# Kernel tuning notes

Measured on AMD Instinct MI355X. Metric: run time of the kernel, lower is better.

Reference implementation:

```python
import jax, jax.numpy as jnp
import numpy as np

EMBED_DIM = 256
HEADS = 8
HEAD_DIM = EMBED_DIM // HEADS
T = 8            # time grid points
N0, N1 = 32, 32  # spatial grid
MAX_PATCH = 16   # static slot budget per cell (last slot = grid latent token)
NEG = -1e30


def construct_grid():
    g0 = jnp.linspace(0.0, 1.0, N0)
    g1 = jnp.linspace(0.0, 1.0, N1)
    G0, G1 = jnp.meshgrid(g0, g1, indexing='ij')
    return jnp.stack([G0, G1], axis=-1)  # [N0, N1, 2]


def setup_inputs() -> dict:
    key = jax.random.key(0)
    ks = jax.random.split(key, 8)
    m, n = 4, 16384
    x = jax.random.uniform(ks[0], (m, n, 3))                       # coords: (time, s0, s1) in [0,1]
    z = jax.random.normal(ks[1], (m, n, EMBED_DIM))
    time_grid = jnp.tile(jnp.linspace(0.0, 1.0, T)[None], (m, 1))  # [m, T] uniform time grid
    latents = jax.random.normal(ks[2], (N0, N1, EMBED_DIM))
    grid = construct_grid()
    s = 1.0 / np.sqrt(EMBED_DIM)
    Wq = jax.random.normal(ks[3], (EMBED_DIM, EMBED_DIM)) * s
    Wk = jax.random.normal(ks[4], (EMBED_DIM, EMBED_DIM)) * s
    Wv = jax.random.normal(ks[5], (EMBED_DIM, EMBED_DIM)) * s
    Wo = jax.random.normal(ks[6], (EMBED_DIM, EMBED_DIM)) * s
    return {'x': x, 'z': z, 'time_grid': time_grid, 'latents': latents,
            'grid': grid, 'Wq': Wq, 'Wk': Wk, 'Wv': Wv, 'Wo': Wo}


def _cumcount(idx):
    # idx: [n] int; returns per-element count of prior occurrences of the same value
    n = idx.shape[0]
    order = jnp.argsort(idx)                 # stable
    srt = idx[order]
    ar = jnp.arange(n)
    is_start = jnp.concatenate([jnp.array([True]), srt[1:] != srt[:-1]])
    seg_start = jax.lax.cummax(jnp.where(is_start, ar, 0), axis=0)
    cc = ar - seg_start
    return jnp.zeros_like(idx).at[order].set(cc.astype(idx.dtype))


def _forward(x, z, time_grid, latents, grid, Wq, Wk, Wv, Wo):
    m, n, _ = x.shape
    t = time_grid.shape[1]
    S = t * N0 * N1
    # --- build x_grid: repeat spatial grid over (m,t), insert time coord at dim 0 ---
    xg_sp = jnp.broadcast_to(grid[None, None], (m, t, N0, N1, 2))
    tg = jnp.broadcast_to(time_grid[:, :, None, None, None], (m, t, N0, N1, 1))
    x_grid = jnp.concatenate([tg, xg_sp], axis=-1)          # [m,t,N0,N1,3]
    # --- nearest gridded neighbour (k=1): per-dim rounding on the regular grid ---
    grid_shape = jnp.array([t, N0, N1], jnp.float32)
    xg_flat = x_grid.reshape(m, S, 3)
    xmin = xg_flat.min(axis=1)                               # [m,3]
    xmax = xg_flat.max(axis=1)
    spacing = (xmax - xmin) / (grid_shape - 1.0)             # [m,3]
    multi = jnp.floor((x - xmin[:, None] + spacing[:, None] / 2) / spacing[:, None])
    multi = jnp.clip(multi, 0.0, grid_shape - 1.0)
    strides = jnp.array([N0 * N1, N1, 1], jnp.float32)
    nearest = jnp.sum(multi * strides, axis=-1).astype(jnp.int32)  # [m,n] flat cell id
    # --- per-cell slot allocation via cumulative count ---
    cum = jax.vmap(_cumcount)(nearest)                       # [m,n]
    P = MAX_PATCH
    valid = cum < (P - 1)                                    # last slot reserved for grid token
    bidx = jnp.arange(m)[:, None]
    cell = jnp.where(valid, nearest, S)                      # out-of-bounds -> dropped
    slot = jnp.minimum(cum, P - 2)
    # --- scatter points into the joint grid [m, S, P, E]; slot P-1 = grid latent ---
    joint = jnp.zeros((m, S, P, EMBED_DIM), z.dtype)
    joint = joint.at[bidx, cell, slot].set(z, mode='drop')
    z_grid_flat = jnp.broadcast_to(
        latents.reshape(1, 1, N0 * N1, EMBED_DIM), (m, t, N0 * N1, EMBED_DIM)
    ).reshape(m, S, EMBED_DIM)
    joint = joint.at[:, :, P - 1].set(z_grid_flat)
    counts = jnp.zeros((m, S), jnp.int32).at[bidx, cell].add(1, mode='drop')
    counts = jnp.minimum(counts, P - 1)
    att_mask = jnp.concatenate(
        [jnp.arange(P - 1)[None, None] < counts[..., None],
         jnp.ones((m, S, 1), bool)], axis=-1)                # [m,S,P]
    # --- masked multi-head cross attention: 1 query (grid latent) per cell ---
    q = (z_grid_flat @ Wq).reshape(m, S, HEADS, HEAD_DIM)
    k = (joint @ Wk).reshape(m, S, P, HEADS, HEAD_DIM)
    v = (joint @ Wv).reshape(m, S, P, HEADS, HEAD_DIM)
    logits = jnp.einsum('mshd,msphd->mshp', q, k) / np.sqrt(HEAD_DIM)
    logits = jnp.where(att_mask[:, :, None, :], logits, NEG)
    attn = jax.nn.softmax(logits, axis=-1)
    out = jnp.einsum('mshp,msphd->mshd', attn, v).reshape(m, S, EMBED_DIM) @ Wo
    z_grid = out.reshape(m, t, N0, N1, EMBED_DIM)
    return x_grid, z_grid


def reference(x, z, time_grid, latents, grid, Wq, Wk, Wv, Wo):
    return _forward(x, z, time_grid, latents, grid, Wq, Wk, Wv, Wo)
```

## Files before the change

### kernel.cpp

```cpp
#include <hip/hip_runtime.h>
#include <hip/hip_bf16.h>

#define T_ 8
#define N0_ 32
#define N1_ 32
#define SP_ (N0_*N1_)
#define S_ (T_*SP_)
#define E_ 256
#define P_ 16
#define NH_ 8
#define HD_ 32

typedef __attribute__((ext_vector_type(8))) short short8;
typedef __attribute__((ext_vector_type(4))) float f32x4;
typedef __attribute__((ext_vector_type(8))) unsigned short u16x8;

__device__ __forceinline__ unsigned short f2bf(float f) {
  __hip_bfloat16 h = __float2bfloat16(f);
  return *reinterpret_cast<unsigned short*>(&h);
}
__device__ __forceinline__ float bf2f(unsigned short u) {
  return __uint_as_float((unsigned)u << 16);
}

__device__ __forceinline__ void gl_lds16(const void* g, void* l) {
  __builtin_amdgcn_global_load_lds(
      (const __attribute__((address_space(1))) unsigned int*)(g),
      (__attribute__((address_space(3))) unsigned int*)(l), 16, 0, 0);
}

__global__ __launch_bounds__(256) void prep(const float* __restrict__ z,
                                            unsigned short* __restrict__ z16,
                                            const float* __restrict__ x,
                                            const float* __restrict__ tg,
                                            const float* __restrict__ grid,
                                            float* __restrict__ out,
                                            int* __restrict__ counts,
                                            int* __restrict__ cell_raw,
                                            const float* __restrict__ Wq,
                                            const float* __restrict__ Wk,
                                            const float* __restrict__ Wv,
                                            const float* __restrict__ Wo,
                                            unsigned short* __restrict__ wT,
                                            const float* __restrict__ latents,
                                            unsigned short* __restrict__ lat16,
                                            int m, int n, int tot_xg, int zn8) {
  __shared__ float ts[64][65];
  __shared__ float st[4][6];
  int bid = blockIdx.x;
  int tid = threadIdx.x;
  if (bid < 2048) {
    for (int i = bid * 256 + tid; i < zn8; i += 2048 * 256) {
      float4 a = *(const float4*)(z + (size_t)i * 8);
      float4 b = *(const float4*)(z + (size_t)i * 8 + 4);
      u16x8 o;
      o[0]=f2bf(a.x); o[1]=f2bf(a.y); o[2]=f2bf(a.z); o[3]=f2bf(a.w);
      o[4]=f2bf(b.x); o[5]=f2bf(b.y); o[6]=f2bf(b.z); o[7]=f2bf(b.w);
      *(u16x8*)(z16 + (size_t)i * 8) = o;
    }
    return;
  }
  if (bid < 2304) {
    if (tid < 64) {
      float mn0 = 1e30f, mx0 = -1e30f, mn1 = 1e30f, mx1 = -1e30f;
      for (int i = tid; i < SP_; i += 64) {
        float g0 = grid[i*2], g1 = grid[i*2+1];
        mn0 = fminf(mn0, g0); mx0 = fmaxf(mx0, g0);
        mn1 = fminf(mn1, g1); mx1 = fmaxf(mx1, g1);
      }
      for (int msk = 32; msk; msk >>= 1) {
        mn0 = fminf(mn0, __shfl_xor(mn0, msk));
        mx0 = fmaxf(mx0, __shfl_xor(mx0, msk));
        mn1 = fminf(mn1, __shfl_xor(mn1, msk));
        mx1 = fmaxf(mx1, __shfl_xor(mx1, msk));
      }
      if (tid == 0) {
        for (int b = 0; b < m; ++b) {
          float tmn = 1e30f, tmx = -1e30f;
          for (int tt = 0; tt < T_; ++tt) {
            float v = tg[b*T_ + tt];
            tmn = fminf(tmn, v); tmx = fmaxf(tmx, v);
          }
          st[b][0] = tmn; st[b][1] = mn0; st[b][2] = mn1;
          st[b][3] = (tmx - tmn) / (float)(T_ - 1);
          st[b][4] = (mx0 - mn0) / (float)(N0_ - 1);
          st[b][5] = (mx1 - mn1) / (float)(N1_ - 1);
        }
      }
    }
    __syncthreads();
    int idx = (bid - 2048) * 256 + tid;
    if (idx < tot_xg) {
      int sp = idx & (SP_ - 1);
      int bt = idx >> 10;
      out[idx*3 + 0] = tg[bt];
      out[idx*3 + 1] = grid[sp*2 + 0];
      out[idx*3 + 2] = grid[sp*2 + 1];
    }
    if (idx < m*n) {
      int b = idx / n;
      int j = idx - b*n;
      const float* s = st[b];
      float xt = x[(size_t)idx*3 + 0], x0 = x[(size_t)idx*3 + 1], x1 = x[(size_t)idx*3 + 2];
      float m0 = floorf((xt - s[0] + s[3]*0.5f) / s[3]);
      float m1 = floorf((x0 - s[1] + s[4]*0.5f) / s[4]);
      float m2 = floorf((x1 - s[2] + s[5]*0.5f) / s[5]);
      m0 = fminf(fmaxf(m0, 0.f), (float)(T_ - 1));
      m1 = fminf(fmaxf(m1, 0.f), (float)(N0_ - 1));
      m2 = fminf(fmaxf(m2, 0.f), (float)(N1_ - 1));
      int sc = (int)m0 * SP_ + (int)m1 * N1_ + (int)m2;
      int cg = b * S_ + sc;
      int old = atomicAdd(&counts[cg], 1);
      if (old < P_) cell_raw[(size_t)cg * P_ + old] = j;
    }
    return;
  }
  if (bid < 2368) {
    int wb = bid - 2304;
    int mat = wb >> 4;
    int tile = wb & 15;
    int tr = (tile >> 2) * 64;
    int tc = (tile & 3) * 64;
    const float* W = mat == 0 ? Wq : mat == 1 ? Wk : mat == 2 ? Wv : Wo;
    int r = tid >> 2, c0 = (tid & 3) * 16;
#pragma unroll
    for (int i = 0; i < 4; ++i) {
      float4 v = *(const float4*)&W[(size_t)(tr + r) * 256 + tc + c0 + i*4];
      ts[r][c0 + i*4 + 0] = v.x; ts[r][c0 + i*4 + 1] = v.y;
      ts[r][c0 + i*4 + 2] = v.z; ts[r][c0 + i*4 + 3] = v.w;
    }
    __syncthreads();
    u16x8 o0, o1;
#pragma unroll
    for (int i = 0; i < 8; ++i) o0[i] = f2bf(ts[c0 + i][r]);
#pragma unroll
    for (int i = 0; i < 8; ++i) o1[i] = f2bf(ts[c0 + 8 + i][r]);
    unsigned short* dst = wT + (size_t)(mat * 256 + tc + r) * 256 + tr + c0;
    *(u16x8*)dst = o0;
    *(u16x8*)(dst + 8) = o1;
    return;
  }
  for (int i = (bid - 2368) * 256 + tid; i < SP_ * E_ / 8; i += 16 * 256) {
    float4 a = *(const float4*)(latents + (size_t)i * 8);
    float4 b = *(const float4*)(latents + (size_t)i * 8 + 4);
    u16x8 o;
    o[0]=f2bf(a.x); o[1]=f2bf(a.y); o[2]=f2bf(a.z); o[3]=f2bf(a.w);
    o[4]=f2bf(b.x); o[5]=f2bf(b.y); o[6]=f2bf(b.z); o[7]=f2bf(b.w);
    *(u16x8*)(lat16 + (size_t)i * 8) = o;
  }
}

template <typename OutT>
__device__ __forceinline__ void g2l_body(unsigned short* __restrict__ ldsbuf,
                                         const unsigned short* __restrict__ A,
                                         const unsigned short* __restrict__ BT,
                                         OutT* __restrict__ C,
                                         int CP, int ldc, int L, int tid) {
  int rp = L / CP, cp = L - rp * CP;

  int wid = tid >> 6, lane = tid & 63, l15 = lane & 15, slot = lane >> 4;
  int wr = (wid >> 1) * 64, wc = (wid & 1) * 64;

  int r8 = lane >> 3, k8 = lane & 7;
  int colsw = (k8 ^ r8) << 3;
  const unsigned short* ga0 = A  + (size_t)(rp * 128 + wid * 32 + r8) * 256 + colsw;
  const unsigned short* gb0 = BT + (size_t)(cp * 128 + wid * 32 + r8) * 256 + colsw;
  unsigned short* As = ldsbuf;
  unsigned short* Bs = ldsbuf + 8192;

  f32x4 acc[4][4] = {};

#pragma unroll
  for (int kt = 0; kt < 4; ++kt) {
    const unsigned short* ga = ga0 + kt * 64;
    const unsigned short* gb = gb0 + kt * 64;
    gl_lds16(ga,          As + (wid*32     ) * 64);
    gl_lds16(ga +  8*256, As + (wid*32 +  8) * 64);
    gl_lds16(ga + 16*256, As + (wid*32 + 16) * 64);
    gl_lds16(ga + 24*256, As + (wid*32 + 24) * 64);
    gl_lds16(gb,          Bs + (wid*32     ) * 64);
    gl_lds16(gb +  8*256, Bs + (wid*32 +  8) * 64);
    gl_lds16(gb + 16*256, Bs + (wid*32 + 16) * 64);
    gl_lds16(gb + 24*256, Bs + (wid*32 + 24) * 64);
    asm volatile("s_waitcnt vmcnt(0)" ::: "memory");
    __builtin_amdgcn_s_barrier();
    asm volatile("" ::: "memory");
#pragma unroll
    for (int kf = 0; kf < 2; ++kf) {
      short8 afr[4], bfr[4];
      int sx = (kf * 4 + slot) ^ (l15 & 7);
#pragma unroll
      for (int mm = 0; mm < 4; ++mm) {
        int row = wr + mm * 16 + l15;
        afr[mm] = *(const short8*)&As[row * 64 + (sx << 3)];
      }
#pragma unroll
      for (int nn = 0; nn < 4; ++nn) {
        int col = wc + nn * 16 + l15;
        bfr[nn] = *(const short8*)&Bs[col * 64 + (sx << 3)];
      }
#pragma unroll
      for (int mm = 0; mm < 4; ++mm)
#pragma unroll
        for (int nn = 0; nn < 4; ++nn)
          acc[mm][nn] = __builtin_amdgcn_mfma_f32_16x16x32_bf16(afr[mm], bfr[nn], acc[mm][nn], 0, 0, 0);
    }
    asm volatile("" ::: "memory");
    __builtin_amdgcn_s_barrier();
    asm volatile("" ::: "memory");
  }

#pragma unroll
  for (int mm = 0; mm < 4; ++mm) {
#pragma unroll
    for (int nn = 0; nn < 4; ++nn) {
      int grow0 = rp * 128 + wr + mm * 16 + slot * 4;
      int gcol  = cp * 128 + wc + nn * 16 + l15;
#pragma unroll
      for (int j = 0; j < 4; ++j) {
        size_t o = (size_t)(grow0 + j) * ldc + gcol;
        if constexpr (__is_same(OutT, float)) C[o] = acc[mm][nn][j];
        else                                  C[o] = __float2bfloat16(acc[mm][nn][j]);
      }
    }
  }
}

__global__ __launch_bounds__(256, 3) void phase2(const unsigned short* __restrict__ z16,
                                                 const unsigned short* __restrict__ wT,
                                                 __hip_bfloat16* __restrict__ kv,
                                                 const unsigned short* __restrict__ lat16,
                                                 float* __restrict__ lat,
                                                 const int* __restrict__ counts,
                                                 int* __restrict__ cell_raw,
                                                 int* __restrict__ pts2, int total) {
  __shared__ unsigned short lds[2 * 128 * 64];
  int bid = blockIdx.x;
  if (bid < 2048) {
    int L = (bid & 7) * 256 + (bid >> 3);
    g2l_body<__hip_bfloat16>(lds, z16, wT + (size_t)256*256, kv, 4, 512, L, threadIdx.x);
    return;
  }
  if (bid < 2096) {
    g2l_body<float>(lds, lat16, wT, lat, 6, 768, bid - 2048, threadIdx.x);
    return;
  }
  int cg = (bid - 2096) * 256 + threadIdx.x;
  if (cg >= total) return;
  int cnt = counts[cg];
  int stored = cnt < P_ ? cnt : P_;
  int eff = cnt < (P_ - 1) ? cnt : (P_ - 1);
  int* p = cell_raw + (size_t)cg * P_;
  for (int i = 1; i < stored; ++i) {
    int key = p[i]; int j = i - 1;
    while (j >= 0 && p[j] > key) { p[j+1] = p[j]; --j; }
    p[j+1] = key;
  }
  int* o = pts2 + (size_t)cg * P_;
  o[0] = eff;
  for (int i = 0; i < eff; ++i) o[1 + i] = p[i];
}

template <typename OutT>
__global__ __launch_bounds__(256, 3) void gemm_g2l(const unsigned short* __restrict__ A,
                                                   const unsigned short* __restrict__ BT,
                                                   OutT* __restrict__ C,
                                                   int CP, int ldc) {
  __shared__ unsigned short lds[2 * 128 * 64];
  int nb = gridDim.x, bid = blockIdx.x;
  int L = bid;
  if ((nb & 7) == 0) L = (bid & 7) * (nb >> 3) + (bid >> 3);
  g2l_body<OutT>(lds, A, BT, C, CP, ldc, L, threadIdx.x);
}

__global__ __launch_bounds__(256) void attn_kernel(
    const float* __restrict__ lat,
    const __hip_bfloat16* __restrict__ kv,
    const int* __restrict__ pts2,
    __hip_bfloat16* __restrict__ attn_out, int n) {
  const float scale = 0.17677669529663687f;
  int wid = threadIdx.x >> 6;
  int lane = threadIdx.x & 63;
  int cellg = blockIdx.x * 4 + wid;
  int b = cellg >> 13;
  int c = cellg & (SP_ - 1);
  int d0 = lane << 2;

  const int* pp = pts2 + (size_t)cellg * P_;
  int4 h0 = *(const int4*)pp;
  int eff = h0.x;

  const float* latc = lat + c * 768 + d0;
  float4 q  = *(const float4*)latc;
  float4 kl = *(const float4*)(latc + 256);
  float4 vl = *(const float4*)(latc + 512);

  float p15 = q.x*kl.x + q.y*kl.y + q.z*kl.z + q.w*kl.w;
  p15 += __shfl_xor(p15, 1);
  p15 += __shfl_xor(p15, 2);
  p15 += __shfl_xor(p15, 4);
  float e15 = __expf(p15 * scale);
  float ssum = e15;
  float4 acc;
  acc.x = e15 * vl.x; acc.y = e15 * vl.y; acc.z = e15 * vl.z; acc.w = e15 * vl.w;

  const unsigned short* kvp = (const unsigned short*)kv;
  size_t bbase = (size_t)b * n;

  int pt[4]; pt[0] = h0.y; pt[1] = h0.z; pt[2] = h0.w; pt[3] = 0;
  int done = 0, cap = 3;
  while (done < eff) {
    int np = eff - done; if (np > cap) np = cap;
    ushort4 kr[4], vr[4];
#pragma unroll
    for (int i = 0; i < 4; ++i) if (i < np) {
      size_t row = (bbase + (size_t)pt[i]) * 512;
      kr[i] = *(const ushort4*)(kvp + row + d0);
      vr[i] = *(const ushort4*)(kvp + row + 256 + d0);
    }
    float e[4];
#pragma unroll
    for (int i = 0; i < 4; ++i) if (i < np) {
      float p = q.x*bf2f(kr[i].x) + q.y*bf2f(kr[i].y) + q.z*bf2f(kr[i].z) + q.w*bf2f(kr[i].w);
      p += __shfl_xor(p, 1);
      p += __shfl_xor(p, 2);
      p += __shfl_xor(p, 4);
      e[i] = __expf(p * scale);
    }
#pragma unroll
    for (int i = 0; i < 4; ++i) if (i < np) {
      ssum += e[i];
      acc.x += e[i] * bf2f(vr[i].x);
      acc.y += e[i] * bf2f(vr[i].y);
      acc.z += e[i] * bf2f(vr[i].z);
      acc.w += e[i] * bf2f(vr[i].w);
    }
    done += np;
    cap = 4;
    if (done < eff) {
      int4 h = *(const int4*)(pp + 1 + done);
      pt[0] = h.x; pt[1] = h.y; pt[2] = h.z; pt[3] = h.w;
    }
  }
  float inv = 1.f / ssum;
  ushort4 o;
  o.x = f2bf(acc.x * inv); o.y = f2bf(acc.y * inv);
  o.z = f2bf(acc.z * inv); o.w = f2bf(acc.w * inv);
  *(ushort4*)((unsigned short*)attn_out + (size_t)cellg * E_ + d0) = o;
}

extern "C" void kernel_launch(void* const* d_in, const int* in_sizes, int n_in,
                              void* d_out, int out_size, void* d_ws, size_t ws_size,
                              hipStream_t stream) {
  const float* x       = (const float*)d_in[0];
  const float* z       = (const float*)d_in[1];
  const float* tg      = (const float*)d_in[2];
  const float* latents = (const float*)d_in[3];
  const float* grid    = (const float*)d_in[4];
  const float* Wq      = (const float*)d_in[5];
  const float* Wk      = (const float*)d_in[6];
  const float* Wv      = (const float*)d_in[7];
  const float* Wo      = (const float*)d_in[8];

  int m = in_sizes[2] / T_;
  int n = in_sizes[1] / (m * E_);
  int MS = m * S_;
  float* out = (float*)d_out;
  int tot_xg = m * T_ * SP_;

  char* w = (char*)d_ws;
  auto alloc = [&](size_t bytes) { char* p = w; w += (bytes + 255) & ~(size_t)255; return p; };
  int*   counts     = (int*)  alloc((size_t)MS * 4);
  int*   cell_raw   = (int*)  alloc((size_t)MS * P_ * 4);
  int*   pts2       = (int*)  alloc((size_t)MS * P_ * 4);
  unsigned short* wT    = (unsigned short*)alloc((size_t)1024 * 256 * 2);
  unsigned short* lat16 = (unsigned short*)alloc((size_t)SP_ * E_ * 2);
  float* lat        = (float*)alloc((size_t)SP_ * 768 * 4);
  __hip_bfloat16* kv       = (__hip_bfloat16*)alloc((size_t)m * n * 512 * 2);
  __hip_bfloat16* attn_out = (__hip_bfloat16*)alloc((size_t)MS * E_ * 2);

  unsigned short* z16 = (unsigned short*)(out + (size_t)tot_xg * 3);

  (void)hipMemsetAsync(counts, 0, (size_t)MS * 4, stream);

  prep<<<2384, 256, 0, stream>>>(z, z16, x, tg, grid, out, counts, cell_raw,
                                 Wq, Wk, Wv, Wo, wT, latents, lat16,
                                 m, n, tot_xg, m * n * E_ / 8);

  phase2<<<2224, 256, 0, stream>>>(z16, wT, kv, lat16, lat, counts, cell_raw, pts2, MS);

  attn_kernel<<<MS/4, 256, 0, stream>>>(lat, kv, pts2, attn_out, n);

  gemm_g2l<float><<<512, 256, 0, stream>>>(
      (const unsigned short*)attn_out, wT + (size_t)768*256, out + (size_t)tot_xg * 3, 2, 256);
}
```

Baseline: 90.95 us.

## Fuse fp32-to-bf16 conversion of z and latents into the projection GEMM loads

Removes the separate pass that converted z (64 MB fp32) and latents to bf16 in the prep kernel. The K/V and latent projection GEMM now loads fp32 A tiles straight into LDS with a swizzled layout and converts them to bf16 in registers before the MFMAs. This saves one full write and re-read of the bf16 copy of z. In exchange the GEMM reads twice as many A bytes, uses more LDS (48KB), and does conversion ALU work in the inner loop with no double buffering.

New measurement: 83.46 us, median of 3. 8.2% less time.

```diff
diff --git a/kernel.cpp b/kernel.cpp
--- a/kernel.cpp
+++ b/kernel.cpp
@@ -29,9 +29,7 @@
       (__attribute__((address_space(3))) unsigned int*)(l), 16, 0, 0);
 }
 
-__global__ __launch_bounds__(256) void prep(const float* __restrict__ z,
-                                            unsigned short* __restrict__ z16,
-                                            const float* __restrict__ x,
+__global__ __launch_bounds__(256) void prep(const float* __restrict__ x,
                                             const float* __restrict__ tg,
                                             const float* __restrict__ grid,
                                             float* __restrict__ out,
@@ -42,25 +40,12 @@
                                             const float* __restrict__ Wv,
                                             const float* __restrict__ Wo,
                                             unsigned short* __restrict__ wT,
-                                            const float* __restrict__ latents,
-                                            unsigned short* __restrict__ lat16,
-                                            int m, int n, int tot_xg, int zn8) {
+                                            int m, int n, int tot_xg) {
   __shared__ float ts[64][65];
   __shared__ float st[4][6];
   int bid = blockIdx.x;
   int tid = threadIdx.x;
-  if (bid < 2048) {
-    for (int i = bid * 256 + tid; i < zn8; i += 2048 * 256) {
-      float4 a = *(const float4*)(z + (size_t)i * 8);
-      float4 b = *(const float4*)(z + (size_t)i * 8 + 4);
-      u16x8 o;
-      o[0]=f2bf(a.x); o[1]=f2bf(a.y); o[2]=f2bf(a.z); o[3]=f2bf(a.w);
-      o[4]=f2bf(b.x); o[5]=f2bf(b.y); o[6]=f2bf(b.z); o[7]=f2bf(b.w);
-      *(u16x8*)(z16 + (size_t)i * 8) = o;
-    }
-    return;
-  }
-  if (bid < 2304) {
+  if (bid < 256) {
     if (tid < 64) {
       float mn0 = 1e30f, mx0 = -1e30f, mn1 = 1e30f, mx1 = -1e30f;
       for (int i = tid; i < SP_; i += 64) {
@@ -89,7 +74,7 @@
       }
     }
     __syncthreads();
-    int idx = (bid - 2048) * 256 + tid;
+    int idx = bid * 256 + tid;
     if (idx < tot_xg) {
       int sp = idx & (SP_ - 1);
       int bt = idx >> 10;
@@ -115,38 +100,110 @@
     }
     return;
   }
-  if (bid < 2368) {
-    int wb = bid - 2304;
-    int mat = wb >> 4;
-    int tile = wb & 15;
-    int tr = (tile >> 2) * 64;
-    int tc = (tile & 3) * 64;
-    const float* W = mat == 0 ? Wq : mat == 1 ? Wk : mat == 2 ? Wv : Wo;
-    int r = tid >> 2, c0 = (tid & 3) * 16;
-#pragma unroll
-    for (int i = 0; i < 4; ++i) {
-      float4 v = *(const float4*)&W[(size_t)(tr + r) * 256 + tc + c0 + i*4];
-      ts[r][c0 + i*4 + 0] = v.x; ts[r][c0 + i*4 + 1] = v.y;
-      ts[r][c0 + i*4 + 2] = v.z; ts[r][c0 + i*4 + 3] = v.w;
-    }
-    __syncthreads();
-    u16x8 o0, o1;
-#pragma unroll
-    for (int i = 0; i < 8; ++i) o0[i] = f2bf(ts[c0 + i][r]);
-#pragma unroll
-    for (int i = 0; i < 8; ++i) o1[i] = f2bf(ts[c0 + 8 + i][r]);
-    unsigned short* dst = wT + (size_t)(mat * 256 + tc + r) * 256 + tr + c0;
-    *(u16x8*)dst = o0;
-    *(u16x8*)(dst + 8) = o1;
-    return;
-  }
-  for (int i = (bid - 2368) * 256 + tid; i < SP_ * E_ / 8; i += 16 * 256) {
-    float4 a = *(const float4*)(latents + (size_t)i * 8);
-    float4 b = *(const float4*)(latents + (size_t)i * 8 + 4);
-    u16x8 o;
-    o[0]=f2bf(a.x); o[1]=f2bf(a.y); o[2]=f2bf(a.z); o[3]=f2bf(a.w);
-    o[4]=f2bf(b.x); o[5]=f2bf(b.y); o[6]=f2bf(b.z); o[7]=f2bf(b.w);
-    *(u16x8*)(lat16 + (size_t)i * 8) = o;
+  int wb = bid - 256;
+  int mat = wb >> 4;
+  int tile = wb & 15;
+  int tr = (tile >> 2) * 64;
+  int tc = (tile & 3) * 64;
+  const float* W = mat == 0 ? Wq : mat == 1 ? Wk : mat == 2 ? Wv : Wo;
+  int r = tid >> 2, c0 = (tid & 3) * 16;
+#pragma unroll
+  for (int i = 0; i < 4; ++i) {
+    float4 v = *(const float4*)&W[(size_t)(tr + r) * 256 + tc + c0 + i*4];
+    ts[r][c0 + i*4 + 0] = v.x; ts[r][c0 + i*4 + 1] = v.y;
+    ts[r][c0 + i*4 + 2] = v.z; ts[r][c0 + i*4 + 3] = v.w;
+  }
+  __syncthreads();
+  u16x8 o0, o1;
+#pragma unroll
+  for (int i = 0; i < 8; ++i) o0[i] = f2bf(ts[c0 + i][r]);
+#pragma unroll
+  for (int i = 0; i < 8; ++i) o1[i] = f2bf(ts[c0 + 8 + i][r]);
+  unsigned short* dst = wT + (size_t)(mat * 256 + tc + r) * 256 + tr + c0;
+  *(u16x8*)dst = o0;
+  *(u16x8*)(dst + 8) = o1;
+}
+
+template <typename OutT>
+__device__ __forceinline__ void f32a_body(char* __restrict__ ldsbuf,
+                                          const float* __restrict__ A,
+                                          const unsigned short* __restrict__ BT,
+                                          OutT* __restrict__ C,
+                                          int CP, int ldc, int L, int tid) {
+  float* As = (float*)ldsbuf;
+  unsigned short* Bs = (unsigned short*)(ldsbuf + 32768);
+  int rp = L / CP, cp = L - rp * CP;
+
+  int wid = tid >> 6, lane = tid & 63, l15 = lane & 15, slot = lane >> 4;
+  int wr = (wid >> 1) * 64, wc = (wid & 1) * 64;
+
+  int arl = lane >> 4, aG = lane & 15;
+  int brl = lane >> 3, bG = lane & 7;
+
+  f32x4 acc[4][4] = {};
+
+#pragma unroll
+  for (int kt = 0; kt < 4; ++kt) {
+#pragma unroll
+    for (int d = 0; d < 8; ++d) {
+      int row = wid * 32 + d * 4 + arl;
+      const float* src = A + (size_t)(rp * 128 + row) * 256 + kt * 64
+                         + (size_t)((aG ^ (row & 15)) << 2);
+      gl_lds16(src, As + (wid * 32 + d * 4) * 64);
+    }
+#pragma unroll
+    for (int d = 0; d < 4; ++d) {
+      int row = wid * 32 + d * 8 + brl;
+      const unsigned short* src = BT + (size_t)(cp * 128 + row) * 256 + kt * 64
+                                  + (size_t)((bG ^ (row & 7)) << 3);
+      gl_lds16(src, Bs + (wid * 32 + d * 8) * 64);
+    }
+    asm volatile("s_waitcnt vmcnt(0)" ::: "memory");
+    __builtin_amdgcn_s_barrier();
+    asm volatile("" ::: "memory");
+#pragma unroll
+    for (int kf = 0; kf < 2; ++kf) {
+      short8 afr[4], bfr[4];
+      int kg = kf * 4 + slot;
+#pragma unroll
+      for (int mm = 0; mm < 4; ++mm) {
+        int row = wr + mm * 16 + l15;
+        f32x4 a0 = *(const f32x4*)&As[row * 64 + (((2 * kg    ) ^ l15) << 2)];
+        f32x4 a1 = *(const f32x4*)&As[row * 64 + (((2 * kg + 1) ^ l15) << 2)];
+        short8 af;
+        af[0]=f2bf(a0[0]); af[1]=f2bf(a0[1]); af[2]=f2bf(a0[2]); af[3]=f2bf(a0[3]);
+        af[4]=f2bf(a1[0]); af[5]=f2bf(a1[1]); af[6]=f2bf(a1[2]); af[7]=f2bf(a1[3]);
+        afr[mm] = af;
+      }
+#pragma unroll
+      for (int nn = 0; nn < 4; ++nn) {
+        int col = wc + nn * 16 + l15;
+        bfr[nn] = *(const short8*)&Bs[col * 64 + ((kg ^ (l15 & 7)) << 3)];
+      }
+#pragma unroll
+      for (int mm = 0; mm < 4; ++mm)
+#pragma unroll
+        for (int nn = 0; nn < 4; ++nn)
+          acc[mm][nn] = __builtin_amdgcn_mfma_f32_16x16x32_bf16(afr[mm], bfr[nn], acc[mm][nn], 0, 0, 0);
+    }
+    asm volatile("" ::: "memory");
+    __builtin_amdgcn_s_barrier();
+    asm volatile("" ::: "memory");
+  }
+
+#pragma unroll
+  for (int mm = 0; mm < 4; ++mm) {
+#pragma unroll
+    for (int nn = 0; nn < 4; ++nn) {
+      int grow0 = rp * 128 + wr + mm * 16 + slot * 4;
+      int gcol  = cp * 128 + wc + nn * 16 + l15;
+#pragma unroll
+      for (int j = 0; j < 4; ++j) {
+        size_t o = (size_t)(grow0 + j) * ldc + gcol;
+        if constexpr (__is_same(OutT, float)) C[o] = acc[mm][nn][j];
+        else                                  C[o] = __float2bfloat16(acc[mm][nn][j]);
+      }
+    }
   }
 }
 
@@ -226,23 +283,23 @@
   }
 }
 
-__global__ __launch_bounds__(256, 3) void phase2(const unsigned short* __restrict__ z16,
+__global__ __launch_bounds__(256, 3) void phase2(const float* __restrict__ z,
                                                  const unsigned short* __restrict__ wT,
                                                  __hip_bfloat16* __restrict__ kv,
-                                                 const unsigned short* __restrict__ lat16,
+                                                 const float* __restrict__ latents,
                                                  float* __restrict__ lat,
                                                  const int* __restrict__ counts,
                                                  int* __restrict__ cell_raw,
                                                  int* __restrict__ pts2, int total) {
-  __shared__ unsigned short lds[2 * 128 * 64];
+  __shared__ char lds[49152];
   int bid = blockIdx.x;
   if (bid < 2048) {
     int L = (bid & 7) * 256 + (bid >> 3);
-    g2l_body<__hip_bfloat16>(lds, z16, wT + (size_t)256*256, kv, 4, 512, L, threadIdx.x);
+    f32a_body<__hip_bfloat16>(lds, z, wT + (size_t)256*256, kv, 4, 512, L, threadIdx.x);
     return;
   }
   if (bid < 2096) {
-    g2l_body<float>(lds, lat16, wT, lat, 6, 768, bid - 2048, threadIdx.x);
+    f32a_body<float>(lds, latents, wT, lat, 6, 768, bid - 2048, threadIdx.x);
     return;
   }
   int cg = (bid - 2096) * 256 + threadIdx.x;
@@ -373,21 +430,17 @@
   int*   counts     = (int*)  alloc((size_t)MS * 4);
   int*   cell_raw   = (int*)  alloc((size_t)MS * P_ * 4);
   int*   pts2       = (int*)  alloc((size_t)MS * P_ * 4);
-  unsigned short* wT    = (unsigned short*)alloc((size_t)1024 * 256 * 2);
-  unsigned short* lat16 = (unsigned short*)alloc((size_t)SP_ * E_ * 2);
+  unsigned short* wT = (unsigned short*)alloc((size_t)1024 * 256 * 2);
   float* lat        = (float*)alloc((size_t)SP_ * 768 * 4);
   __hip_bfloat16* kv       = (__hip_bfloat16*)alloc((size_t)m * n * 512 * 2);
   __hip_bfloat16* attn_out = (__hip_bfloat16*)alloc((size_t)MS * E_ * 2);
 
-  unsigned short* z16 = (unsigned short*)(out + (size_t)tot_xg * 3);
-
   (void)hipMemsetAsync(counts, 0, (size_t)MS * 4, stream);
 
-  prep<<<2384, 256, 0, stream>>>(z, z16, x, tg, grid, out, counts, cell_raw,
-                                 Wq, Wk, Wv, Wo, wT, latents, lat16,
-                                 m, n, tot_xg, m * n * E_ / 8);
-
-  phase2<<<2224, 256, 0, stream>>>(z16, wT, kv, lat16, lat, counts, cell_raw, pts2, MS);
+  prep<<<320, 256, 0, stream>>>(x, tg, grid, out, counts, cell_raw,
+                                Wq, Wk, Wv, Wo, wT, m, n, tot_xg);
+
+  phase2<<<2224, 256, 0, stream>>>(z, wT, kv, latents, lat, counts, cell_raw, pts2, MS);
 
   attn_kernel<<<MS/4, 256, 0, stream>>>(lat, kv, pts2, attn_out, n);
 
```
